# Performance work log

Measured on AMD Instinct MI355X. Metric: run time of the kernel, lower is better.

Reference implementation:

```python
import jax, jax.numpy as jnp
import numpy as np
from jax import lax

H, W = 26, 26          # largest feature-map size for resnet18(2,3) @ 224 after AvgPool2d(3,1)
D = 384                # 128 + 256 concatenated channels
M = 200000             # coreset memory-bank size
IMG = 224
K = 5
SIGMA = 4.0
KS = 2 * int(4.0 * SIGMA + 0.5) + 1  # 33, torchvision-style gaussian blur kernel


def _l2_normalize(x, eps=1e-12):
    n = jnp.linalg.norm(x, axis=-1, keepdims=True)
    return x / jnp.maximum(n, eps)


def _gaussian_kernel1d():
    r = (KS - 1) // 2
    x = jnp.arange(-r, r + 1, dtype=jnp.float32)
    k = jnp.exp(-0.5 * (x / SIGMA) ** 2)
    return k / jnp.sum(k)


def _gaussian_blur(x):
    # x: [1,1,IMG,IMG]; separable gaussian with reflect padding
    k = _gaussian_kernel1d()
    r = (KS - 1) // 2
    x = jnp.pad(x, ((0, 0), (0, 0), (r, r), (r, r)), mode='reflect')
    kh = k.reshape(1, 1, KS, 1)
    kw = k.reshape(1, 1, 1, KS)
    x = lax.conv_general_dilated(x, kh, (1, 1), 'VALID')
    x = lax.conv_general_dilated(x, kw, (1, 1), 'VALID')
    return x


def setup_inputs() -> dict:
    key = jax.random.key(0)
    k1, k2 = jax.random.split(key)
    patch = jax.random.normal(k1, (H * W, D), dtype=jnp.float32)
    patch_lib = _l2_normalize(jax.random.normal(k2, (M, D), dtype=jnp.float32))
    return {"patch": patch, "patch_lib": patch_lib}


def reference(patch, patch_lib):
    # patch: [N, D] raw concatenated features; patch_lib: [M, D] (pre-normalized at fit time)
    patch = _l2_normalize(patch)  # F.normalize(patch, p=2, dim=1)

    # torch.cdist(patch, patch_lib) via ||a||^2 + ||b||^2 - 2 a.b
    pn = jnp.sum(patch * patch, axis=1, keepdims=True)      # [N,1]
    ln = jnp.sum(patch_lib * patch_lib, axis=1)             # [M]
    d2 = pn + ln[None, :] - 2.0 * (patch @ patch_lib.T)     # [N,M]
    dist = jnp.sqrt(jnp.maximum(d2, 0.0))

    min_val = jnp.min(dist, axis=1)                         # [N]
    min_idx = jnp.argmin(dist, axis=1)                      # [N]
    s_idx = jnp.argmax(min_val)
    s_star = min_val[s_idx]

    m_test_star = patch[s_idx]                              # [D]
    m_star = patch_lib[min_idx[s_idx]]                      # [D]

    # cdist(m_star, patch_lib) + topk(k=5, largest=False)
    d_star2 = ln + jnp.sum(m_star * m_star) - 2.0 * (patch_lib @ m_star)  # [M]
    d_star = jnp.sqrt(jnp.maximum(d_star2, 0.0))
    _, nn_idx = lax.top_k(-d_star, K)
    nb_vectors = patch_lib[nn_idx]                          # [K, D]
    nb_dists = jnp.linalg.norm(m_test_star[None, :] - nb_vectors, axis=1)

    numerator = jnp.exp(jnp.linalg.norm(m_test_star - m_star))
    denominator = jnp.sum(jnp.exp(nb_dists))
    w = 1.0 - numerator / denominator
    s = w * s_star

    s_map = min_val.reshape(1, 1, H, W)
    # F.interpolate bilinear, align_corners=False == half-pixel linear resize
    s_map = jax.image.resize(s_map, (1, 1, IMG, IMG), method='linear')
    s_map = _gaussian_blur(s_map)
    return s, s_map
```

## Files before the change

### kernel.cpp

```cpp
#include <hip/hip_runtime.h>
#include <stdint.h>

#define NP    676
#define NPAD  768
#define DD    384
#define MM    200000
#define IMG   224

typedef unsigned int u32;
typedef unsigned long long u64;
typedef short bf16x8 __attribute__((ext_vector_type(8)));
typedef float f32x4 __attribute__((ext_vector_type(4)));

#define WS_PACKED   0u
#define WS_SCAL     6144u
#define WS_MV       6400u
#define WS_TOPS     9728u
#define WS_PNORM    15360u
#define WS_PNB      1195008u
#define WS_DSTAR    1784832u
#define WS_BUFA     3384832u
#define WS_BUFB     3585536u

__device__ inline unsigned short f2bf(float f) {
  u32 u = __float_as_uint(f);
  u += 0x7FFFu + ((u >> 16) & 1u);
  return (unsigned short)(u >> 16);
}

__device__ __forceinline__ u32 cvtpk(float lo, float hi) {
  u32 r;
  asm("v_cvt_pk_bf16_f32 %0, %1, %2" : "=v"(r) : "v"(lo), "v"(hi));
  return r;
}

__device__ __forceinline__ void gld16(const void* g, void* l) {
  __builtin_amdgcn_global_load_lds((const __attribute__((address_space(1))) u32*)g,
                                   (__attribute__((address_space(3))) u32*)l, 16, 0, 0);
}

__global__ void k_norm(const float* __restrict__ patch, float* __restrict__ pnorm,
                       unsigned short* __restrict__ pnb, u64* __restrict__ packed_) {
  __shared__ float red[2];
  __shared__ float scs;
  int i = blockIdx.x, t = threadIdx.x;
  if (i < 6) packed_[i * 128 + t] = 0ull;
  if (i >= NP) {
    for (int j = 0; j < 3; ++j) {
      pnorm[(size_t)i * DD + t + 128 * j] = 0.f;
      pnb[(size_t)i * DD + t + 128 * j] = 0;
    }
    return;
  }
  float x0 = patch[(size_t)i * DD + t];
  float x1 = patch[(size_t)i * DD + t + 128];
  float x2 = patch[(size_t)i * DD + t + 256];
  float s = x0 * x0 + x1 * x1 + x2 * x2;
#pragma unroll
  for (int m = 1; m < 64; m <<= 1) s += __shfl_xor(s, m, 64);
  if ((t & 63) == 0) red[t >> 6] = s;
  __syncthreads();
  if (t == 0) scs = 1.f / fmaxf(sqrtf(red[0] + red[1]), 1e-12f);
  __syncthreads();
  float k = scs;
  pnorm[(size_t)i * DD + t]       = x0 * k;
  pnorm[(size_t)i * DD + t + 128] = x1 * k;
  pnorm[(size_t)i * DD + t + 256] = x2 * k;
  pnb[(size_t)i * DD + t]       = f2bf(x0 * k);
  pnb[(size_t)i * DD + t + 128] = f2bf(x1 * k);
  pnb[(size_t)i * DD + t + 256] = f2bf(x2 * k);
}

__global__ __launch_bounds__(256, 2) void k_pass1(const unsigned short* __restrict__ pnb,
                                                  const float* __restrict__ lib,
                                                  u64* __restrict__ packed_) {
  __shared__ __align__(16) unsigned short bt[2 * 6144];
  const int t = threadIdx.x;
  const int xcd = blockIdx.x & 7;
  const int idx = blockIdx.x >> 3;
  const int logical = (xcd < 4 ? xcd * 587 : 4 * 587 + (xcd - 4) * 586) + idx;
  const int cc = logical / 6, rg = logical - cc * 6;
  const int col0 = cc * 256;
  const int rowbase = rg * 128;
  const int wave = t >> 6, lane = t & 63;
  const int quad = lane >> 4, l15 = lane & 15;
  const int nchunk = (MM - col0 < 256) ? (MM - col0) / 16 : 16;

  u32 srcoff[3], wdst[3];
#pragma unroll
  for (int it = 0; it < 3; ++it) {
    int s = it * 256 + t;
    int r = s / 48, u = s - r * 48;
    srcoff[it] = (u32)(r * 1536 + u * 32);
    wdst[it]   = (u32)(r * 768 + ((u ^ (r & 7)) << 4));
  }
  int bo[12];
#pragma unroll
  for (int kt = 0; kt < 12; ++kt)
    bo[kt] = l15 * 768 + (((quad + 4 * kt) ^ (l15 & 7)) << 4);

  bf16x8 areg[2][12];
  {
    u32 soffA[6];
#pragma unroll
    for (int it = 0; it < 6; ++it) {
      int s = (wave * 6 + it) * 64 + lane;
      int r = s / 48, u = s - r * 48;
      soffA[it] = (u32)(r * 768 + ((u ^ (r & 7)) << 4));
    }
#pragma unroll
    for (int q = 0; q < 4; ++q) {
      if (q) __syncthreads();
      const char* srcb = (const char*)pnb + (size_t)(rowbase + q * 32) * 768;
#pragma unroll
      for (int it = 0; it < 6; ++it)
        gld16(srcb + soffA[it], (char*)bt + (wave * 6 + it) * 1024);
      __syncthreads();
      if (wave == q) {
#pragma unroll
        for (int mi = 0; mi < 2; ++mi)
#pragma unroll
          for (int kt = 0; kt < 12; ++kt)
            areg[mi][kt] = *(const bf16x8*)((const char*)bt +
                            (size_t)(mi * 16 + l15) * 768 +
                            (((quad + 4 * kt) ^ (l15 & 7)) << 4));
      }
    }
  }
  __syncthreads();

  u32 best[8];
#pragma unroll
  for (int j = 0; j < 8; ++j) best[j] = 0u;

  const char* bsrc = (const char*)lib + (size_t)col0 * 1536;
  float4 preg[3][2];

  {
#pragma unroll
    for (int it = 0; it < 3; ++it) {
      preg[it][0] = *(const float4*)(bsrc + srcoff[it]);
      preg[it][1] = *(const float4*)(bsrc + srcoff[it] + 16);
    }
#pragma unroll
    for (int it = 0; it < 3; ++it) {
      uint4 o;
      o.x = cvtpk(preg[it][0].x, preg[it][0].y);
      o.y = cvtpk(preg[it][0].z, preg[it][0].w);
      o.z = cvtpk(preg[it][1].x, preg[it][1].y);
      o.w = cvtpk(preg[it][1].z, preg[it][1].w);
      *(uint4*)((char*)bt + wdst[it]) = o;
    }
    if (nchunk > 1) {
      const char* s1 = bsrc + 24576;
#pragma unroll
      for (int it = 0; it < 3; ++it) {
        preg[it][0] = *(const float4*)(s1 + srcoff[it]);
        preg[it][1] = *(const float4*)(s1 + srcoff[it] + 16);
      }
    }
  }

  int cur = 0;
#pragma unroll 1
  for (int c = 0; c < nchunk; ++c) {
    __syncthreads();
    if (c + 1 < nchunk) {
#pragma unroll
      for (int it = 0; it < 3; ++it) {
        uint4 o;
        o.x = cvtpk(preg[it][0].x, preg[it][0].y);
        o.y = cvtpk(preg[it][0].z, preg[it][0].w);
        o.z = cvtpk(preg[it][1].x, preg[it][1].y);
        o.w = cvtpk(preg[it][1].z, preg[it][1].w);
        *(uint4*)((char*)bt + (cur ^ 1) * 12288 + wdst[it]) = o;
      }
    }
    if (c + 2 < nchunk) {
      const char* s2 = bsrc + (size_t)(c + 2) * 24576;
#pragma unroll
      for (int it = 0; it < 3; ++it) {
        preg[it][0] = *(const float4*)(s2 + srcoff[it]);
        preg[it][1] = *(const float4*)(s2 + srcoff[it] + 16);
      }
    }
    const char* bufb = (const char*)bt + cur * 12288;
    f32x4 acc[2];
#pragma unroll
    for (int mi = 0; mi < 2; ++mi) {
      acc[mi][0] = 0.f; acc[mi][1] = 0.f; acc[mi][2] = 0.f; acc[mi][3] = 0.f;
    }
#pragma unroll
    for (int kt = 0; kt < 12; ++kt) {
      bf16x8 bf = *(const bf16x8*)(bufb + bo[kt]);
#pragma unroll
      for (int mi = 0; mi < 2; ++mi)
        acc[mi] = __builtin_amdgcn_mfma_f32_16x16x32_bf16(areg[mi][kt], bf, acc[mi], 0, 0, 0);
    }
    const u32 colbits = 255u - (u32)(c * 16 + l15);
#pragma unroll
    for (int mi = 0; mi < 2; ++mi)
#pragma unroll
      for (int r = 0; r < 4; ++r) {
        u32 kb = __float_as_uint(acc[mi][r] + 3.0f);
        u32 k = (kb & 0xFFFFFF00u) | colbits;
        if (k > best[mi * 4 + r]) best[mi * 4 + r] = k;
      }
    cur ^= 1;
  }

#pragma unroll
  for (int mi = 0; mi < 2; ++mi)
#pragma unroll
    for (int r = 0; r < 4; ++r) {
      u32 k = best[mi * 4 + r];
#pragma unroll
      for (int m = 1; m < 16; m <<= 1) {
        u32 o = (u32)__shfl_xor((int)k, m, 64);
        k = o > k ? o : k;
      }
      if (l15 == 0) {
        int col = col0 + 255 - (int)(k & 255u);
        int row = rowbase + wave * 32 + mi * 16 + quad * 4 + r;
        u64 g = ((u64)(k & 0xFFFFFF00u) << 32) | (u64)(0xFFFFFFFFu - (u32)col);
        atomicMax(&packed_[row], g);
      }
    }
}

__global__ void k_select(const u64* __restrict__ packed_, u32* __restrict__ scal,
                         float* __restrict__ mv) {
  __shared__ u64 red[256];
  int t = threadIdx.x;
  u64 best = 0ull;
  for (int i = t; i < NP; i += 256) {
    u64 p = packed_[i];
    float d = __uint_as_float((u32)(p >> 32)) - 3.0f;
    float dist = sqrtf(fmaxf(2.f - 2.f * d, 0.f));
    mv[i] = dist;
    u64 key = ((u64)__float_as_uint(dist) << 32) | (u32)(0xFFFFFFFFu - (u32)i);
    if (key > best) best = key;
  }
  red[t] = best;
  __syncthreads();
  for (int s = 128; s > 0; s >>= 1) {
    if (t < s && red[t + s] > red[t]) red[t] = red[t + s];
    __syncthreads();
  }
  if (t == 0) {
    u64 k = red[0];
    u32 sidx = 0xFFFFFFFFu - (u32)k;
    u64 p = packed_[sidx];
    u32 jstar = 0xFFFFFFFFu - (u32)p;
    scal[0] = sidx;
    scal[1] = jstar;
    ((float*)scal)[2] = __uint_as_float((u32)(k >> 32));
  }
}

__global__ void k_dstar(const float* __restrict__ lib, const u32* __restrict__ scal,
                        u64* __restrict__ dstar) {
  int gid = blockIdx.x * 256 + threadIdx.x;
  int w = gid >> 6, lane = gid & 63;
  int quad = lane >> 4, l15 = lane & 15;
  u32 jstar = scal[1];
  const float4* ms = (const float4*)(lib + (size_t)jstar * DD);
  float4 mf[6];
#pragma unroll
  for (int j = 0; j < 6; ++j) mf[j] = ms[j * 16 + l15];
  for (int r4 = w; r4 < 50000; r4 += 3200) {
    int row = r4 * 4 + quad;
    const float4* xr = (const float4*)(lib + (size_t)row * DD);
    float dot = 0.f;
#pragma unroll
    for (int j = 0; j < 6; ++j) {
      float4 u = xr[j * 16 + l15];
      dot += mf[j].x * u.x + mf[j].y * u.y + mf[j].z * u.z + mf[j].w * u.w;
    }
#pragma unroll
    for (int mm = 1; mm < 16; mm <<= 1) dot += __shfl_xor(dot, mm, 64);
    if (l15 == 0) {
      float dist = sqrtf(fmaxf(2.f - 2.f * dot, 0.f));
      dstar[row] = ((u64)__float_as_uint(dist) << 32) | (u32)row;
    }
  }
}

__device__ inline void merge5(const u64* a, const u64* b, u64* o) {
  int ia = 0, ib = 0;
#pragma unroll
  for (int j = 0; j < 5; ++j) {
    u64 va = a[ia], vb = b[ib];
    if (va <= vb) { o[j] = va; ++ia; } else { o[j] = vb; ++ib; }
  }
}

__global__ void k_top5a(const u64* __restrict__ dstar, u64* __restrict__ tops) {
  __shared__ u64 l[256 * 5];
  int t = threadIdx.x, b = blockIdx.x;
  int start = b * 1563;
  int end = start + 1563; if (end > MM) end = MM;
  u64 a0 = ~0ull, a1 = ~0ull, a2 = ~0ull, a3 = ~0ull, a4 = ~0ull;
  for (int i = start + t; i < end; i += 256) {
    u64 v = dstar[i];
    if (v < a4) {
      if (v < a0)      { a4 = a3; a3 = a2; a2 = a1; a1 = a0; a0 = v; }
      else if (v < a1) { a4 = a3; a3 = a2; a2 = a1; a1 = v; }
      else if (v < a2) { a4 = a3; a3 = a2; a2 = v; }
      else if (v < a3) { a4 = a3; a3 = v; }
      else             { a4 = v; }
    }
  }
  l[t * 5 + 0] = a0; l[t * 5 + 1] = a1; l[t * 5 + 2] = a2; l[t * 5 + 3] = a3; l[t * 5 + 4] = a4;
  __syncthreads();
  for (int s = 128; s > 0; s >>= 1) {
    if (t < s) {
      u64 o[5];
      merge5(&l[t * 5], &l[(t + s) * 5], o);
#pragma unroll
      for (int j = 0; j < 5; ++j) l[t * 5 + j] = o[j];
    }
    __syncthreads();
  }
  if (t < 5) tops[b * 5 + t] = l[t];
}

__global__ void k_final(const u64* __restrict__ tops, const u32* __restrict__ scal,
                        const float* __restrict__ pnorm, const float* __restrict__ lib,
                        float* __restrict__ out) {
  __shared__ u64 l[128 * 5];
  __shared__ u32 nn[5];
  int t = threadIdx.x;
  if (t < 128) {
#pragma unroll
    for (int j = 0; j < 5; ++j) l[t * 5 + j] = tops[t * 5 + j];
  }
  __syncthreads();
  for (int s = 64; s > 0; s >>= 1) {
    if (t < s) {
      u64 o[5];
      merge5(&l[t * 5], &l[(t + s) * 5], o);
#pragma unroll
      for (int j = 0; j < 5; ++j) l[t * 5 + j] = o[j];
    }
    __syncthreads();
  }
  if (t < 5) nn[t] = (u32)l[t];
  __syncthreads();
  if (t < 64) {
    int lane = t;
    u32 sidx = scal[0], jstar = scal[1];
    const float* mt = pnorm + (size_t)sidx * DD;
    float mtv[6];
#pragma unroll
    for (int r = 0; r < 6; ++r) mtv[r] = mt[lane + 64 * r];
    float dist[6];
    for (int n = 0; n < 6; ++n) {
      u32 idx = (n == 0) ? jstar : nn[n - 1];
      const float* v = lib + (size_t)idx * DD;
      float p = 0.f;
#pragma unroll
      for (int r = 0; r < 6; ++r) {
        float d = mtv[r] - v[lane + 64 * r];
        p += d * d;
      }
#pragma unroll
      for (int m = 1; m < 64; m <<= 1) p += __shfl_xor(p, m, 64);
      dist[n] = sqrtf(p);
    }
    if (lane == 0) {
      float nrm = dist[0];
      float den = 0.f;
      for (int n = 1; n < 6; ++n) den += expf(dist[n]);
      out[0] = (1.f - expf(nrm) / den) * nrm;
    }
  }
}

__global__ void k_resize(const float* __restrict__ mv, float* __restrict__ A) {
  int i = blockIdx.x * 256 + threadIdx.x;
  int Y = i / IMG, X = i - Y * IMG;
  const float sc = 26.f / 224.f;
  float sy = (Y + 0.5f) * sc - 0.5f;
  float sx = (X + 0.5f) * sc - 0.5f;
  float fy = sy - floorf(sy), fx = sx - floorf(sx);
  int y0 = (int)floorf(sy), x0 = (int)floorf(sx);
  int y1 = y0 + 1, x1 = x0 + 1;
  y0 = min(max(y0, 0), 25); y1 = min(max(y1, 0), 25);
  x0 = min(max(x0, 0), 25); x1 = min(max(x1, 0), 25);
  float v00 = mv[y0 * 26 + x0], v01 = mv[y0 * 26 + x1];
  float v10 = mv[y1 * 26 + x0], v11 = mv[y1 * 26 + x1];
  A[i] = (1.f - fy) * ((1.f - fx) * v00 + fx * v01) + fy * ((1.f - fx) * v10 + fx * v11);
}

__global__ void k_blurh(const float* __restrict__ A, float* __restrict__ B) {
  __shared__ float kw[33];
  __shared__ float kinv;
  int t = threadIdx.x;
  if (t < 33) {
    float x = ((float)t - 16.f) * 0.25f;
    kw[t] = expf(-0.5f * x * x);
  }
  __syncthreads();
  if (t == 0) {
    float s = 0.f;
    for (int j = 0; j < 33; ++j) s += kw[j];
    kinv = 1.f / s;
  }
  __syncthreads();
  int i = blockIdx.x * 256 + t;
  int Y = i / IMG, X = i - Y * IMG;
  float s = 0.f;
  for (int j = 0; j < 33; ++j) {
    int xx = X + j - 16;
    xx = xx < 0 ? -xx : (xx > 223 ? 446 - xx : xx);
    s += kw[j] * A[Y * IMG + xx];
  }
  B[i] = s * kinv;
}

__global__ void k_blurv(const float* __restrict__ B, float* __restrict__ out) {
  __shared__ float kw[33];
  __shared__ float kinv;
  int t = threadIdx.x;
  if (t < 33) {
    float x = ((float)t - 16.f) * 0.25f;
    kw[t] = expf(-0.5f * x * x);
  }
  __syncthreads();
  if (t == 0) {
    float s = 0.f;
    for (int j = 0; j < 33; ++j) s += kw[j];
    kinv = 1.f / s;
  }
  __syncthreads();
  int i = blockIdx.x * 256 + t;
  int Y = i / IMG, X = i - Y * IMG;
  float s = 0.f;
  for (int j = 0; j < 33; ++j) {
    int yy = Y + j - 16;
    yy = yy < 0 ? -yy : (yy > 223 ? 446 - yy : yy);
    s += kw[j] * B[yy * IMG + X];
  }
  out[1 + i] = s * kinv;
}

extern "C" void kernel_launch(void* const* d_in, const int* in_sizes, int n_in,
                              void* d_out, int out_size, void* d_ws, size_t ws_size,
                              hipStream_t stream) {
  const float* patch = (const float*)d_in[0];
  const float* lib   = (const float*)d_in[1];
  float* out = (float*)d_out;
  char* w = (char*)d_ws;

  u64*  packed_ = (u64*)(w + WS_PACKED);
  u32*  scal    = (u32*)(w + WS_SCAL);
  float* mv     = (float*)(w + WS_MV);
  u64*  tops    = (u64*)(w + WS_TOPS);
  float* pnorm  = (float*)(w + WS_PNORM);
  unsigned short* pnb  = (unsigned short*)(w + WS_PNB);
  u64*  dstar   = (u64*)(w + WS_DSTAR);
  float* bufA   = (float*)(w + WS_BUFA);
  float* bufB   = (float*)(w + WS_BUFB);

  k_norm  <<<NPAD, 128, 0, stream>>>(patch, pnorm, pnb, packed_);
  k_pass1 <<<4692, 256, 0, stream>>>(pnb, lib, packed_);
  k_select<<<1,    256, 0, stream>>>(packed_, scal, mv);
  k_dstar <<<800,  256, 0, stream>>>(lib, scal, dstar);
  k_top5a <<<128,  256, 0, stream>>>(dstar, tops);
  k_final <<<1,    256, 0, stream>>>(tops, scal, pnorm, lib, out);
  k_resize<<<196,  256, 0, stream>>>(mv, bufA);
  k_blurh <<<196,  256, 0, stream>>>(bufA, bufB);
  k_blurv <<<196,  256, 0, stream>>>(bufB, out);
}
```

Baseline: 586.4 us.

## Deepen global prefetch to three chunks and replace syncthreads with LDS-only barrier

```diff
diff --git a/kernel.cpp b/kernel.cpp
--- a/kernel.cpp
+++ b/kernel.cpp
@@ -134,80 +134,98 @@
   for (int j = 0; j < 8; ++j) best[j] = 0u;
 
   const char* bsrc = (const char*)lib + (size_t)col0 * 1536;
-  float4 preg[3][2];
+  float4 pregA[3][2], pregB[3][2];
 
   {
 #pragma unroll
     for (int it = 0; it < 3; ++it) {
-      preg[it][0] = *(const float4*)(bsrc + srcoff[it]);
-      preg[it][1] = *(const float4*)(bsrc + srcoff[it] + 16);
+      pregA[it][0] = *(const float4*)(bsrc + srcoff[it]);
+      pregA[it][1] = *(const float4*)(bsrc + srcoff[it] + 16);
+    }
+#pragma unroll
+    for (int it = 0; it < 3; ++it) {
+      pregB[it][0] = *(const float4*)(bsrc + 24576 + srcoff[it]);
+      pregB[it][1] = *(const float4*)(bsrc + 24576 + srcoff[it] + 16);
     }
 #pragma unroll
     for (int it = 0; it < 3; ++it) {
       uint4 o;
-      o.x = cvtpk(preg[it][0].x, preg[it][0].y);
-      o.y = cvtpk(preg[it][0].z, preg[it][0].w);
-      o.z = cvtpk(preg[it][1].x, preg[it][1].y);
-      o.w = cvtpk(preg[it][1].z, preg[it][1].w);
+      o.x = cvtpk(pregA[it][0].x, pregA[it][0].y);
+      o.y = cvtpk(pregA[it][0].z, pregA[it][0].w);
+      o.z = cvtpk(pregA[it][1].x, pregA[it][1].y);
+      o.w = cvtpk(pregA[it][1].z, pregA[it][1].w);
       *(uint4*)((char*)bt + wdst[it]) = o;
     }
-    if (nchunk > 1) {
-      const char* s1 = bsrc + 24576;
+    if (2 < nchunk) {
+      const char* s2 = bsrc + 2 * 24576;
 #pragma unroll
       for (int it = 0; it < 3; ++it) {
-        preg[it][0] = *(const float4*)(s1 + srcoff[it]);
-        preg[it][1] = *(const float4*)(s1 + srcoff[it] + 16);
+        pregA[it][0] = *(const float4*)(s2 + srcoff[it]);
+        pregA[it][1] = *(const float4*)(s2 + srcoff[it] + 16);
       }
     }
+    asm volatile("s_waitcnt lgkmcnt(0)" ::: "memory");
+    __builtin_amdgcn_s_barrier();
+    __builtin_amdgcn_sched_barrier(0);
   }
 
   int cur = 0;
+#define PASS_ITER(c, PW, PL)                                                   \
+  {                                                                            \
+    if ((c) + 1 < nchunk) {                                                    \
+      _Pragma("unroll")                                                        \
+      for (int it = 0; it < 3; ++it) {                                         \
+        uint4 o;                                                               \
+        o.x = cvtpk(PW[it][0].x, PW[it][0].y);                                 \
+        o.y = cvtpk(PW[it][0].z, PW[it][0].w);                                 \
+        o.z = cvtpk(PW[it][1].x, PW[it][1].y);                                 \
+        o.w = cvtpk(PW[it][1].z, PW[it][1].w);                                 \
+        *(uint4*)((char*)bt + (cur ^ 1) * 12288 + wdst[it]) = o;               \
+      }                                                                        \
+    }                                                                          \
+    if ((c) + 3 < nchunk) {                                                    \
+      const char* s3 = bsrc + (size_t)((c) + 3) * 24576;                       \
+      _Pragma("unroll")                                                        \
+      for (int it = 0; it < 3; ++it) {                                         \
+        PL[it][0] = *(const float4*)(s3 + srcoff[it]);                         \
+        PL[it][1] = *(const float4*)(s3 + srcoff[it] + 16);                    \
+      }                                                                        \
+    }                                                                          \
+    const char* bufb = (const char*)bt + cur * 12288;                          \
+    f32x4 acc[2];                                                              \
+    _Pragma("unroll")                                                          \
+    for (int mi = 0; mi < 2; ++mi) {                                           \
+      acc[mi][0] = 0.f; acc[mi][1] = 0.f; acc[mi][2] = 0.f; acc[mi][3] = 0.f;  \
+    }                                                                          \
+    _Pragma("unroll")                                                          \
+    for (int kt = 0; kt < 12; ++kt) {                                          \
+      bf16x8 bf = *(const bf16x8*)(bufb + bo[kt]);                             \
+      _Pragma("unroll")                                                        \
+      for (int mi = 0; mi < 2; ++mi)                                           \
+        acc[mi] = __builtin_amdgcn_mfma_f32_16x16x32_bf16(areg[mi][kt], bf,    \
+                                                          acc[mi], 0, 0, 0);  \
+    }                                                                          \
+    const u32 colbits = 255u - (u32)((c) * 16 + l15);                          \
+    _Pragma("unroll")                                                          \
+    for (int mi = 0; mi < 2; ++mi)                                             \
+      _Pragma("unroll")                                                        \
+      for (int r = 0; r < 4; ++r) {                                            \
+        u32 kb = __float_as_uint(acc[mi][r] + 3.0f);                           \
+        u32 k = (kb & 0xFFFFFF00u) | colbits;                                  \
+        if (k > best[mi * 4 + r]) best[mi * 4 + r] = k;                        \
+      }                                                                        \
+    asm volatile("s_waitcnt lgkmcnt(0)" ::: "memory");                         \
+    __builtin_amdgcn_s_barrier();                                              \
+    __builtin_amdgcn_sched_barrier(0);                                         \
+    cur ^= 1;                                                                  \
+  }
+
 #pragma unroll 1
-  for (int c = 0; c < nchunk; ++c) {
-    __syncthreads();
-    if (c + 1 < nchunk) {
-#pragma unroll
-      for (int it = 0; it < 3; ++it) {
-        uint4 o;
-        o.x = cvtpk(preg[it][0].x, preg[it][0].y);
-        o.y = cvtpk(preg[it][0].z, preg[it][0].w);
-        o.z = cvtpk(preg[it][1].x, preg[it][1].y);
-        o.w = cvtpk(preg[it][1].z, preg[it][1].w);
-        *(uint4*)((char*)bt + (cur ^ 1) * 12288 + wdst[it]) = o;
-      }
-    }
-    if (c + 2 < nchunk) {
-      const char* s2 = bsrc + (size_t)(c + 2) * 24576;
-#pragma unroll
-      for (int it = 0; it < 3; ++it) {
-        preg[it][0] = *(const float4*)(s2 + srcoff[it]);
-        preg[it][1] = *(const float4*)(s2 + srcoff[it] + 16);
-      }
-    }
-    const char* bufb = (const char*)bt + cur * 12288;
-    f32x4 acc[2];
-#pragma unroll
-    for (int mi = 0; mi < 2; ++mi) {
-      acc[mi][0] = 0.f; acc[mi][1] = 0.f; acc[mi][2] = 0.f; acc[mi][3] = 0.f;
-    }
-#pragma unroll
-    for (int kt = 0; kt < 12; ++kt) {
-      bf16x8 bf = *(const bf16x8*)(bufb + bo[kt]);
-#pragma unroll
-      for (int mi = 0; mi < 2; ++mi)
-        acc[mi] = __builtin_amdgcn_mfma_f32_16x16x32_bf16(areg[mi][kt], bf, acc[mi], 0, 0, 0);
-    }
-    const u32 colbits = 255u - (u32)(c * 16 + l15);
-#pragma unroll
-    for (int mi = 0; mi < 2; ++mi)
-#pragma unroll
-      for (int r = 0; r < 4; ++r) {
-        u32 kb = __float_as_uint(acc[mi][r] + 3.0f);
-        u32 k = (kb & 0xFFFFFF00u) | colbits;
-        if (k > best[mi * 4 + r]) best[mi * 4 + r] = k;
-      }
-    cur ^= 1;
-  }
+  for (int c = 0; c < nchunk; c += 2) {
+    PASS_ITER(c, pregB, pregB);
+    PASS_ITER(c + 1, pregA, pregA);
+  }
+#undef PASS_ITER
 
 #pragma unroll
   for (int mi = 0; mi < 2; ++mi)
```

Result: no change. 587.7 us (+0.2%).
